# Kernel optimization log

Measured on AMD Instinct MI355X. Metric: run time of the kernel, lower is better.

The kernel has to match this reference:

```python
import jax, jax.numpy as jnp
import numpy as np

BATCH, SEQ, DMODEL, DHID = 4, 4096, 1024, 1024
R_MIN, R_MAX = 0.9, 0.99
MAX_PHASE = np.pi / 50  # module overrides ctor arg with pi/50
EPS = 1e-5


def setup_inputs() -> dict:
    key = jax.random.key(0)
    ks = jax.random.split(key, 8)
    # nu_init
    u1 = jax.random.uniform(ks[0], (DHID,)) * (1 - EPS) + EPS
    mag_sq = u1 * (R_MAX ** 2 - R_MIN ** 2) + R_MIN ** 2
    nu_log = jnp.log(-0.5 * jnp.log(mag_sq + EPS))
    # theta_init
    u2 = jax.random.uniform(ks[1], (DHID,)) * (1 - EPS) + EPS
    theta_log = jnp.log(MAX_PHASE * u2)
    B_re = jax.random.normal(ks[2], (DHID, DMODEL)) / np.sqrt(2 * DMODEL)
    B_im = jax.random.normal(ks[3], (DHID, DMODEL)) / np.sqrt(2 * DMODEL)
    C_re = jax.random.normal(ks[4], (DMODEL, DHID)) / np.sqrt(DHID)
    C_im = jax.random.normal(ks[5], (DMODEL, DHID)) / np.sqrt(DHID)
    D_skip = jax.random.normal(ks[6], (DMODEL,))
    inputs = jax.random.normal(ks[7], (BATCH, SEQ, DMODEL), dtype=jnp.float32)
    return {"inputs": inputs, "nu_log": nu_log, "theta_log": theta_log,
            "B_re": B_re, "B_im": B_im, "C_re": C_re, "C_im": C_im,
            "D_skip": D_skip}


def reference(inputs, nu_log, theta_log, B_re, B_im, C_re, C_im, D_skip):
    nu = jnp.exp(nu_log)
    theta = jnp.exp(theta_log)
    diag_lambda = jnp.exp(-nu + 1j * theta)            # [H] complex
    # forward recomputes gamma_log from nu_log (parameter gamma_log unused)
    gamma_log = 0.5 * jnp.log(1 - jnp.exp(-2 * jnp.exp(nu_log)) + EPS)
    B_norm = (B_re + 1j * B_im) * jnp.exp(gamma_log)[:, None]  # [H, D]
    inputs_c = inputs.astype(jnp.complex64)
    Bu = jnp.einsum('hd,btd->bth', B_norm, inputs_c)   # [B, T, H]

    def step(h, bu_t):
        h = diag_lambda * h + bu_t
        return h, h

    h0 = jnp.zeros((inputs.shape[0], diag_lambda.shape[0]), dtype=Bu.dtype)
    _, hs = jax.lax.scan(step, h0, jnp.swapaxes(Bu, 0, 1))  # [T, B, H]
    hs = jnp.swapaxes(hs, 0, 1)                              # [B, T, H]
    C_complex = C_re + 1j * C_im                              # [D, H]
    out = jnp.einsum('bth,dh->btd', hs, C_complex).real + inputs * D_skip
    return out.astype(jnp.float32)
```

## Files before the change

kernel.cpp:

```cpp
#include <hip/hip_runtime.h>


typedef __bf16 bf16x8 __attribute__((ext_vector_type(8)));
typedef float floatx4 __attribute__((ext_vector_type(4)));

__device__ __forceinline__ unsigned short f2bf(float f) {
  unsigned u = __float_as_uint(f);
  u += 0x7fffu + ((u >> 16) & 1u);
  return (unsigned short)(u >> 16);
}
__device__ __forceinline__ float bf2f(unsigned short s) {
  return __uint_as_float(((unsigned)s) << 16);
}


__global__ void prep_params(const float* __restrict__ nu_log,
                            const float* __restrict__ theta_log,
                            float* __restrict__ lam,
                            float* __restrict__ lamL,
                            float* __restrict__ gamma)
{
  int h = blockIdx.x * 256 + threadIdx.x;
  float nu = expf(nu_log[h]);
  float th = expf(theta_log[h]);
  float r = expf(-nu);
  lam[h]        = r * cosf(th);
  lam[1024 + h] = r * sinf(th);
  float rL = expf(-128.0f * nu);
  lamL[h]        = rL * cosf(128.0f * th);
  lamL[1024 + h] = rL * sinf(128.0f * th);
  gamma[h] = sqrtf(1.0f - expf(-2.0f * nu) + 1e-5f);
}

__global__ void prep_B(const float* __restrict__ B_re, const float* __restrict__ B_im,
                       const float* __restrict__ gamma, unsigned short* __restrict__ Bcat)
{
  int tid = blockIdx.x * 256 + threadIdx.x;
  int n = tid >> 10;
  int d = tid & 1023;
  int h = n & 1023;
  float v = (n < 1024 ? B_re[h * 1024 + d] : B_im[h * 1024 + d]) * gamma[h];
  Bcat[tid] = f2bf(v);
}

__global__ void prep_C(const float* __restrict__ C_re, const float* __restrict__ C_im,
                       unsigned short* __restrict__ Ccat)
{
  int tid = blockIdx.x * 256 + threadIdx.x;
  int d = tid >> 11;
  int k = tid & 2047;
  float v = (k < 1024) ? C_re[d * 1024 + k] : -C_im[d * 1024 + (k - 1024)];
  Ccat[tid] = f2bf(v);
}

__global__ void conv_inputs(const float* __restrict__ in, unsigned short* __restrict__ outb)
{
  int tid = blockIdx.x * 256 + threadIdx.x;
  float4 v = ((const float4*)in)[tid];
  unsigned lo = (unsigned)f2bf(v.x) | ((unsigned)f2bf(v.y) << 16);
  unsigned hi = (unsigned)f2bf(v.z) | ((unsigned)f2bf(v.w) << 16);
  ((uint2*)outb)[tid] = make_uint2(lo, hi);
}


template <int EPI>
__global__ __launch_bounds__(256) void gemm_bt_kernel(
    const unsigned short* __restrict__ A,
    const unsigned short* __restrict__ Bt,
    void* __restrict__ Cout,
    int M, int N, int K,
    const float* __restrict__ skip_in,
    const float* __restrict__ skip_w)
{
  __shared__ unsigned short As[2][128 * 32];
  __shared__ unsigned short Bs[2][128 * 32];

  const int tid  = threadIdx.x;
  const int lane = tid & 63;
  const int wave = tid >> 6;
  const int wm = wave >> 1;
  const int wn = wave & 1;

  const int flat    = blockIdx.x;
  const int xcd     = flat & 7;
  const int local   = flat >> 3;
  const int m_tile  = xcd * 16 + (local & 15);
  const int n_tile  = local >> 4;
  const int m0 = m_tile * 128;
  const int n0 = n_tile * 128;

  const int ldr = lane >> 2;
  const int pos = lane & 3;
  const int lm  = lane & 15;
  const int q   = lane >> 4;

  const int r0 = wave * 32 + ldr;
  const int ca0 = pos ^ ((r0 >> 1) & 3);
  const int r1 = r0 + 16;
  const int ca1 = pos ^ ((r1 >> 1) & 3);

  const unsigned short* gA0 = A  + (size_t)(m0 + r0) * K + ca0 * 8;
  const unsigned short* gA1 = A  + (size_t)(m0 + r1) * K + ca1 * 8;
  const unsigned short* gB0 = Bt + (size_t)(n0 + r0) * K + ca0 * 8;
  const unsigned short* gB1 = Bt + (size_t)(n0 + r1) * K + ca1 * 8;
  const int lofs0 = r0 * 32 + pos * 8;
  const int lofs1 = r1 * 32 + pos * 8;

  floatx4 acc[4][4];
#pragma unroll
  for (int i = 0; i < 4; ++i)
#pragma unroll
    for (int j = 0; j < 4; ++j)
      acc[i][j] = (floatx4){0.f, 0.f, 0.f, 0.f};

  {
    __builtin_amdgcn_global_load_lds(
        (const __attribute__((address_space(1))) void*)gA0,
        (__attribute__((address_space(3))) void*)&As[0][lofs0], 16, 0, 0);
    __builtin_amdgcn_global_load_lds(
        (const __attribute__((address_space(1))) void*)gA1,
        (__attribute__((address_space(3))) void*)&As[0][lofs1], 16, 0, 0);
    __builtin_amdgcn_global_load_lds(
        (const __attribute__((address_space(1))) void*)gB0,
        (__attribute__((address_space(3))) void*)&Bs[0][lofs0], 16, 0, 0);
    __builtin_amdgcn_global_load_lds(
        (const __attribute__((address_space(1))) void*)gB1,
        (__attribute__((address_space(3))) void*)&Bs[0][lofs1], 16, 0, 0);
  }

  int cur = 0;
  for (int kt = 0; kt < K; kt += 32) {
    __syncthreads();

    const int nxt = cur ^ 1;
    if (kt + 32 < K) {
      const int ko = kt + 32;
      __builtin_amdgcn_global_load_lds(
          (const __attribute__((address_space(1))) void*)(gA0 + ko),
          (__attribute__((address_space(3))) void*)&As[nxt][lofs0], 16, 0, 0);
      __builtin_amdgcn_global_load_lds(
          (const __attribute__((address_space(1))) void*)(gA1 + ko),
          (__attribute__((address_space(3))) void*)&As[nxt][lofs1], 16, 0, 0);
      __builtin_amdgcn_global_load_lds(
          (const __attribute__((address_space(1))) void*)(gB0 + ko),
          (__attribute__((address_space(3))) void*)&Bs[nxt][lofs0], 16, 0, 0);
      __builtin_amdgcn_global_load_lds(
          (const __attribute__((address_space(1))) void*)(gB1 + ko),
          (__attribute__((address_space(3))) void*)&Bs[nxt][lofs1], 16, 0, 0);
    }

    bf16x8 afrag[4], bfrag[4];
#pragma unroll
    for (int i = 0; i < 4; ++i) {
      const int r = wm * 64 + i * 16 + lm;
      afrag[i] = *reinterpret_cast<const bf16x8*>(&As[cur][r * 32 + (q ^ ((r >> 1) & 3)) * 8]);
    }
#pragma unroll
    for (int j = 0; j < 4; ++j) {
      const int r = wn * 64 + j * 16 + lm;
      bfrag[j] = *reinterpret_cast<const bf16x8*>(&Bs[cur][r * 32 + (q ^ ((r >> 1) & 3)) * 8]);
    }
#pragma unroll
    for (int i = 0; i < 4; ++i)
#pragma unroll
      for (int j = 0; j < 4; ++j)
        acc[i][j] = __builtin_amdgcn_mfma_f32_16x16x32_bf16(afrag[i], bfrag[j], acc[i][j], 0, 0, 0);

    cur = nxt;
  }

#pragma unroll
  for (int i = 0; i < 4; ++i) {
#pragma unroll
    for (int j = 0; j < 4; ++j) {
      const int row0 = m0 + wm * 64 + i * 16 + q * 4;
      const int col  = n0 + wn * 64 + j * 16 + lm;
#pragma unroll
      for (int r = 0; r < 4; ++r) {
        const size_t idx = (size_t)(row0 + r) * N + col;
        if (EPI == 0) {
          ((unsigned short*)Cout)[idx] = f2bf(acc[i][j][r]);
        } else {
          ((float*)Cout)[idx] = acc[i][j][r] + skip_in[idx] * skip_w[col];
        }
      }
    }
  }
}


__global__ void scan_finals(const unsigned short* __restrict__ Bu,
                            const float* __restrict__ lam,
                            float2* __restrict__ finals)
{
  int tid = blockIdx.x * 256 + threadIdx.x;
  int h = tid & 1023, c = (tid >> 10) & 31, b = tid >> 15;
  float lre = lam[h], lim = lam[1024 + h];
  const unsigned short* p = Bu + ((size_t)(b * 4096 + c * 128) * 2048) + h;
  float yre = 0.f, yim = 0.f;
#pragma unroll 4
  for (int t = 0; t < 128; ++t) {
    float ure = bf2f(p[0]);
    float uim = bf2f(p[1024]);
    float nre = fmaf(lre, yre, fmaf(-lim, yim, ure));
    float nim = fmaf(lre, yim, fmaf(lim, yre, uim));
    yre = nre; yim = nim;
    p += 2048;
  }
  finals[tid] = make_float2(yre, yim);
}

__global__ void scan_carries(const float2* __restrict__ finals,
                             const float* __restrict__ lamL,
                             float2* __restrict__ carry)
{
  int tid = blockIdx.x * 256 + threadIdx.x;
  int h = tid & 1023, b = tid >> 10;
  float Lre = lamL[h], Lim = lamL[1024 + h];
  float Hre = 0.f, Him = 0.f;
  for (int c = 0; c < 32; ++c) {
    size_t i = ((size_t)(b * 32 + c) << 10) + h;
    carry[i] = make_float2(Hre, Him);
    float2 f = finals[i];
    float nre = fmaf(Lre, Hre, fmaf(-Lim, Him, f.x));
    float nim = fmaf(Lre, Him, fmaf(Lim, Hre, f.y));
    Hre = nre; Him = nim;
  }
}

__global__ void scan_apply(const float* __restrict__ lam,
                           const float2* __restrict__ carry,
                           unsigned short* __restrict__ Bu)
{
  int tid = blockIdx.x * 256 + threadIdx.x;
  int h = tid & 1023, c = (tid >> 10) & 31, b = tid >> 15;
  float lre = lam[h], lim = lam[1024 + h];
  float2 cv = carry[tid];
  float yre = cv.x, yim = cv.y;
  unsigned short* p = Bu + ((size_t)(b * 4096 + c * 128) * 2048) + h;
#pragma unroll 4
  for (int t = 0; t < 128; ++t) {
    float ure = bf2f(p[0]);
    float uim = bf2f(p[1024]);
    float nre = fmaf(lre, yre, fmaf(-lim, yim, ure));
    float nim = fmaf(lre, yim, fmaf(lim, yre, uim));
    yre = nre; yim = nim;
    p[0]    = f2bf(yre);
    p[1024] = f2bf(yim);
    p += 2048;
  }
}


extern "C" void kernel_launch(void* const* d_in, const int* in_sizes, int n_in,
                              void* d_out, int out_size, void* d_ws, size_t ws_size,
                              hipStream_t stream)
{
  const float* inputs    = (const float*)d_in[0];
  const float* nu_log    = (const float*)d_in[1];
  const float* theta_log = (const float*)d_in[2];
  const float* B_re      = (const float*)d_in[3];
  const float* B_im      = (const float*)d_in[4];
  const float* C_re      = (const float*)d_in[5];
  const float* C_im      = (const float*)d_in[6];
  const float* D_skip    = (const float*)d_in[7];
  float* out = (float*)d_out;

  char* ws = (char*)d_ws;
  float* lam   = (float*)ws;
  float* lamL  = lam + 2048;
  float* gamma = lamL + 2048;
  unsigned short* inp_bf = (unsigned short*)(ws + (1 << 16));
  unsigned short* Bcat   = inp_bf + (size_t)16384 * 1024;
  unsigned short* Ccat   = Bcat   + (size_t)2048 * 1024;
  unsigned short* Bu     = Ccat   + (size_t)1024 * 2048;
  float2* finals = (float2*)(Bu + (size_t)16384 * 2048);
  float2* carry  = finals + 131072;

  prep_params<<<4,    256, 0, stream>>>(nu_log, theta_log, lam, lamL, gamma);
  prep_B     <<<8192, 256, 0, stream>>>(B_re, B_im, gamma, Bcat);
  prep_C     <<<8192, 256, 0, stream>>>(C_re, C_im, Ccat);
  conv_inputs<<<16384,256, 0, stream>>>(inputs, inp_bf);

  gemm_bt_kernel<0><<<2048, 256, 0, stream>>>(
      inp_bf, Bcat, Bu, 16384, 2048, 1024, nullptr, nullptr);

  scan_finals <<<512, 256, 0, stream>>>(Bu, lam, finals);
  scan_carries<<<16,  256, 0, stream>>>(finals, lamL, carry);
  scan_apply  <<<512, 256, 0, stream>>>(lam, carry, Bu);

  gemm_bt_kernel<1><<<1024, 256, 0, stream>>>(
      Bu, Ccat, out, 16384, 1024, 2048, inputs, D_skip);
}
```

Measured before the change: 364.2 us.

## Fuse prep kernels, load GEMM A fragments directly, vectorize scan kernels

Merges the four preprocessing kernels into one launch, with gamma computed inline per B element. The GEMM kernel now reads its A operand fragments straight from global memory into registers, skipping the LDS staging for A. The scan kernels handle four hidden channels per thread using 8-byte packed bf16 loads and stores, with a quarter of the blocks. This cuts launches, LDS traffic and per-element load count, but risks uncoalesced, unprefetched A reads in the GEMMs and lower occupancy in the scans (only 128 blocks).

Result: slower. 515.1 us (+41.4%).

```diff
diff --git a/kernel.cpp b/kernel.cpp
--- a/kernel.cpp
+++ b/kernel.cpp
@@ -14,52 +14,51 @@
 }
 
 
-__global__ void prep_params(const float* __restrict__ nu_log,
-                            const float* __restrict__ theta_log,
-                            float* __restrict__ lam,
-                            float* __restrict__ lamL,
-                            float* __restrict__ gamma)
-{
-  int h = blockIdx.x * 256 + threadIdx.x;
-  float nu = expf(nu_log[h]);
-  float th = expf(theta_log[h]);
-  float r = expf(-nu);
-  lam[h]        = r * cosf(th);
-  lam[1024 + h] = r * sinf(th);
-  float rL = expf(-128.0f * nu);
-  lamL[h]        = rL * cosf(128.0f * th);
-  lamL[1024 + h] = rL * sinf(128.0f * th);
-  gamma[h] = sqrtf(1.0f - expf(-2.0f * nu) + 1e-5f);
-}
-
-__global__ void prep_B(const float* __restrict__ B_re, const float* __restrict__ B_im,
-                       const float* __restrict__ gamma, unsigned short* __restrict__ Bcat)
-{
-  int tid = blockIdx.x * 256 + threadIdx.x;
-  int n = tid >> 10;
-  int d = tid & 1023;
-  int h = n & 1023;
-  float v = (n < 1024 ? B_re[h * 1024 + d] : B_im[h * 1024 + d]) * gamma[h];
-  Bcat[tid] = f2bf(v);
-}
-
-__global__ void prep_C(const float* __restrict__ C_re, const float* __restrict__ C_im,
-                       unsigned short* __restrict__ Ccat)
-{
-  int tid = blockIdx.x * 256 + threadIdx.x;
-  int d = tid >> 11;
-  int k = tid & 2047;
-  float v = (k < 1024) ? C_re[d * 1024 + k] : -C_im[d * 1024 + (k - 1024)];
-  Ccat[tid] = f2bf(v);
-}
-
-__global__ void conv_inputs(const float* __restrict__ in, unsigned short* __restrict__ outb)
-{
-  int tid = blockIdx.x * 256 + threadIdx.x;
-  float4 v = ((const float4*)in)[tid];
-  unsigned lo = (unsigned)f2bf(v.x) | ((unsigned)f2bf(v.y) << 16);
-  unsigned hi = (unsigned)f2bf(v.z) | ((unsigned)f2bf(v.w) << 16);
-  ((uint2*)outb)[tid] = make_uint2(lo, hi);
+__global__ void prep_fused(const float* __restrict__ nu_log,
+                           const float* __restrict__ theta_log,
+                           const float* __restrict__ B_re,
+                           const float* __restrict__ B_im,
+                           const float* __restrict__ C_re,
+                           const float* __restrict__ C_im,
+                           const float* __restrict__ inputs,
+                           float* __restrict__ lam,
+                           float* __restrict__ lamL,
+                           unsigned short* __restrict__ Bcat,
+                           unsigned short* __restrict__ Ccat,
+                           unsigned short* __restrict__ inp_bf)
+{
+  const int bx = blockIdx.x;
+  if (bx < 16384) {
+    int tid = bx * 256 + threadIdx.x;
+    float4 v = ((const float4*)inputs)[tid];
+    unsigned lo = (unsigned)f2bf(v.x) | ((unsigned)f2bf(v.y) << 16);
+    unsigned hi = (unsigned)f2bf(v.z) | ((unsigned)f2bf(v.w) << 16);
+    ((uint2*)inp_bf)[tid] = make_uint2(lo, hi);
+  } else if (bx < 24576) {
+    int tid = (bx - 16384) * 256 + threadIdx.x;
+    int n = tid >> 10;
+    int d = tid & 1023;
+    int h = n & 1023;
+    float gamma = sqrtf(1.0f - expf(-2.0f * expf(nu_log[h])) + 1e-5f);
+    float v = (n < 1024 ? B_re[h * 1024 + d] : B_im[h * 1024 + d]) * gamma;
+    Bcat[tid] = f2bf(v);
+  } else if (bx < 32768) {
+    int tid = (bx - 24576) * 256 + threadIdx.x;
+    int d = tid >> 11;
+    int k = tid & 2047;
+    float v = (k < 1024) ? C_re[d * 1024 + k] : -C_im[d * 1024 + (k - 1024)];
+    Ccat[tid] = f2bf(v);
+  } else {
+    int h = (bx - 32768) * 256 + threadIdx.x;
+    float nu = expf(nu_log[h]);
+    float th = expf(theta_log[h]);
+    float r = expf(-nu);
+    lam[h]        = r * cosf(th);
+    lam[1024 + h] = r * sinf(th);
+    float rL = expf(-128.0f * nu);
+    lamL[h]        = rL * cosf(128.0f * th);
+    lamL[1024 + h] = rL * sinf(128.0f * th);
+  }
 }
 
 
@@ -72,7 +71,6 @@
     const float* __restrict__ skip_in,
     const float* __restrict__ skip_w)
 {
-  __shared__ unsigned short As[2][128 * 32];
   __shared__ unsigned short Bs[2][128 * 32];
 
   const int tid  = threadIdx.x;
@@ -98,14 +96,13 @@
   const int ca0 = pos ^ ((r0 >> 1) & 3);
   const int r1 = r0 + 16;
   const int ca1 = pos ^ ((r1 >> 1) & 3);
-
-  const unsigned short* gA0 = A  + (size_t)(m0 + r0) * K + ca0 * 8;
-  const unsigned short* gA1 = A  + (size_t)(m0 + r1) * K + ca1 * 8;
   const unsigned short* gB0 = Bt + (size_t)(n0 + r0) * K + ca0 * 8;
   const unsigned short* gB1 = Bt + (size_t)(n0 + r1) * K + ca1 * 8;
   const int lofs0 = r0 * 32 + pos * 8;
   const int lofs1 = r1 * 32 + pos * 8;
 
+  const unsigned short* gAf = A + (size_t)(m0 + wm * 64 + lm) * K + q * 8;
+
   floatx4 acc[4][4];
 #pragma unroll
   for (int i = 0; i < 4; ++i)
@@ -113,20 +110,12 @@
     for (int j = 0; j < 4; ++j)
       acc[i][j] = (floatx4){0.f, 0.f, 0.f, 0.f};
 
-  {
-    __builtin_amdgcn_global_load_lds(
-        (const __attribute__((address_space(1))) void*)gA0,
-        (__attribute__((address_space(3))) void*)&As[0][lofs0], 16, 0, 0);
-    __builtin_amdgcn_global_load_lds(
-        (const __attribute__((address_space(1))) void*)gA1,
-        (__attribute__((address_space(3))) void*)&As[0][lofs1], 16, 0, 0);
-    __builtin_amdgcn_global_load_lds(
-        (const __attribute__((address_space(1))) void*)gB0,
-        (__attribute__((address_space(3))) void*)&Bs[0][lofs0], 16, 0, 0);
-    __builtin_amdgcn_global_load_lds(
-        (const __attribute__((address_space(1))) void*)gB1,
-        (__attribute__((address_space(3))) void*)&Bs[0][lofs1], 16, 0, 0);
-  }
+  __builtin_amdgcn_global_load_lds(
+      (const __attribute__((address_space(1))) void*)gB0,
+      (__attribute__((address_space(3))) void*)&Bs[0][lofs0], 16, 0, 0);
+  __builtin_amdgcn_global_load_lds(
+      (const __attribute__((address_space(1))) void*)gB1,
+      (__attribute__((address_space(3))) void*)&Bs[0][lofs1], 16, 0, 0);
 
   int cur = 0;
   for (int kt = 0; kt < K; kt += 32) {
@@ -135,12 +124,6 @@
     const int nxt = cur ^ 1;
     if (kt + 32 < K) {
       const int ko = kt + 32;
-      __builtin_amdgcn_global_load_lds(
-          (const __attribute__((address_space(1))) void*)(gA0 + ko),
-          (__attribute__((address_space(3))) void*)&As[nxt][lofs0], 16, 0, 0);
-      __builtin_amdgcn_global_load_lds(
-          (const __attribute__((address_space(1))) void*)(gA1 + ko),
-          (__attribute__((address_space(3))) void*)&As[nxt][lofs1], 16, 0, 0);
       __builtin_amdgcn_global_load_lds(
           (const __attribute__((address_space(1))) void*)(gB0 + ko),
           (__attribute__((address_space(3))) void*)&Bs[nxt][lofs0], 16, 0, 0);
@@ -149,17 +132,18 @@
           (__attribute__((address_space(3))) void*)&Bs[nxt][lofs1], 16, 0, 0);
     }
 
-    bf16x8 afrag[4], bfrag[4];
-#pragma unroll
-    for (int i = 0; i < 4; ++i) {
-      const int r = wm * 64 + i * 16 + lm;
-      afrag[i] = *reinterpret_cast<const bf16x8*>(&As[cur][r * 32 + (q ^ ((r >> 1) & 3)) * 8]);
-    }
+    bf16x8 afrag[4];
+#pragma unroll
+    for (int i = 0; i < 4; ++i)
+      afrag[i] = *reinterpret_cast<const bf16x8*>(gAf + (size_t)i * 16 * K + kt);
+
+    bf16x8 bfrag[4];
 #pragma unroll
     for (int j = 0; j < 4; ++j) {
       const int r = wn * 64 + j * 16 + lm;
       bfrag[j] = *reinterpret_cast<const bf16x8*>(&Bs[cur][r * 32 + (q ^ ((r >> 1) & 3)) * 8]);
     }
+
 #pragma unroll
     for (int i = 0; i < 4; ++i)
 #pragma unroll
@@ -194,20 +178,31 @@
                             float2* __restrict__ finals)
 {
   int tid = blockIdx.x * 256 + threadIdx.x;
-  int h = tid & 1023, c = (tid >> 10) & 31, b = tid >> 15;
-  float lre = lam[h], lim = lam[1024 + h];
-  const unsigned short* p = Bu + ((size_t)(b * 4096 + c * 128) * 2048) + h;
-  float yre = 0.f, yim = 0.f;
-#pragma unroll 4
+  int h4 = (tid & 255) * 4, c = (tid >> 8) & 31, b = tid >> 13;
+  float lre[4], lim[4], yre[4], yim[4];
+#pragma unroll
+  for (int j = 0; j < 4; ++j) {
+    lre[j] = lam[h4 + j]; lim[j] = lam[1024 + h4 + j];
+    yre[j] = 0.f; yim[j] = 0.f;
+  }
+  const unsigned short* p = Bu + ((size_t)(b * 4096 + c * 128) * 2048) + h4;
+#pragma unroll 2
   for (int t = 0; t < 128; ++t) {
-    float ure = bf2f(p[0]);
-    float uim = bf2f(p[1024]);
-    float nre = fmaf(lre, yre, fmaf(-lim, yim, ure));
-    float nim = fmaf(lre, yim, fmaf(lim, yre, uim));
-    yre = nre; yim = nim;
+    uint2 ur = *(const uint2*)(p);
+    uint2 ui = *(const uint2*)(p + 1024);
+    float re[4] = {bf2f(ur.x & 0xffff), bf2f(ur.x >> 16), bf2f(ur.y & 0xffff), bf2f(ur.y >> 16)};
+    float im[4] = {bf2f(ui.x & 0xffff), bf2f(ui.x >> 16), bf2f(ui.y & 0xffff), bf2f(ui.y >> 16)};
+#pragma unroll
+    for (int j = 0; j < 4; ++j) {
+      float nre = fmaf(lre[j], yre[j], fmaf(-lim[j], yim[j], re[j]));
+      float nim = fmaf(lre[j], yim[j], fmaf(lim[j], yre[j], im[j]));
+      yre[j] = nre; yim[j] = nim;
+    }
     p += 2048;
   }
-  finals[tid] = make_float2(yre, yim);
+  float2* f = finals + ((size_t)(b * 32 + c) << 10) + h4;
+#pragma unroll
+  for (int j = 0; j < 4; ++j) f[j] = make_float2(yre[j], yim[j]);
 }
 
 __global__ void scan_carries(const float2* __restrict__ finals,
@@ -233,20 +228,35 @@
                            unsigned short* __restrict__ Bu)
 {
   int tid = blockIdx.x * 256 + threadIdx.x;
-  int h = tid & 1023, c = (tid >> 10) & 31, b = tid >> 15;
-  float lre = lam[h], lim = lam[1024 + h];
-  float2 cv = carry[tid];
-  float yre = cv.x, yim = cv.y;
-  unsigned short* p = Bu + ((size_t)(b * 4096 + c * 128) * 2048) + h;
-#pragma unroll 4
+  int h4 = (tid & 255) * 4, c = (tid >> 8) & 31, b = tid >> 13;
+  float lre[4], lim[4], yre[4], yim[4];
+  const float2* cv = carry + ((size_t)(b * 32 + c) << 10) + h4;
+#pragma unroll
+  for (int j = 0; j < 4; ++j) {
+    lre[j] = lam[h4 + j]; lim[j] = lam[1024 + h4 + j];
+    float2 v = cv[j];
+    yre[j] = v.x; yim[j] = v.y;
+  }
+  unsigned short* p = Bu + ((size_t)(b * 4096 + c * 128) * 2048) + h4;
+#pragma unroll 2
   for (int t = 0; t < 128; ++t) {
-    float ure = bf2f(p[0]);
-    float uim = bf2f(p[1024]);
-    float nre = fmaf(lre, yre, fmaf(-lim, yim, ure));
-    float nim = fmaf(lre, yim, fmaf(lim, yre, uim));
-    yre = nre; yim = nim;
-    p[0]    = f2bf(yre);
-    p[1024] = f2bf(yim);
+    uint2 ur = *(const uint2*)(p);
+    uint2 ui = *(const uint2*)(p + 1024);
+    float re[4] = {bf2f(ur.x & 0xffff), bf2f(ur.x >> 16), bf2f(ur.y & 0xffff), bf2f(ur.y >> 16)};
+    float im[4] = {bf2f(ui.x & 0xffff), bf2f(ui.x >> 16), bf2f(ui.y & 0xffff), bf2f(ui.y >> 16)};
+#pragma unroll
+    for (int j = 0; j < 4; ++j) {
+      float nre = fmaf(lre[j], yre[j], fmaf(-lim[j], yim[j], re[j]));
+      float nim = fmaf(lre[j], yim[j], fmaf(lim[j], yre[j], im[j]));
+      yre[j] = nre; yim[j] = nim;
+    }
+    uint2 sr, si;
+    sr.x = (unsigned)f2bf(yre[0]) | ((unsigned)f2bf(yre[1]) << 16);
+    sr.y = (unsigned)f2bf(yre[2]) | ((unsigned)f2bf(yre[3]) << 16);
+    si.x = (unsigned)f2bf(yim[0]) | ((unsigned)f2bf(yim[1]) << 16);
+    si.y = (unsigned)f2bf(yim[2]) | ((unsigned)f2bf(yim[3]) << 16);
+    *(uint2*)(p) = sr;
+    *(uint2*)(p + 1024) = si;
     p += 2048;
   }
 }
@@ -269,7 +279,6 @@
   char* ws = (char*)d_ws;
   float* lam   = (float*)ws;
   float* lamL  = lam + 2048;
-  float* gamma = lamL + 2048;
   unsigned short* inp_bf = (unsigned short*)(ws + (1 << 16));
   unsigned short* Bcat   = inp_bf + (size_t)16384 * 1024;
   unsigned short* Ccat   = Bcat   + (size_t)2048 * 1024;
@@ -277,17 +286,15 @@
   float2* finals = (float2*)(Bu + (size_t)16384 * 2048);
   float2* carry  = finals + 131072;
 
-  prep_params<<<4,    256, 0, stream>>>(nu_log, theta_log, lam, lamL, gamma);
-  prep_B     <<<8192, 256, 0, stream>>>(B_re, B_im, gamma, Bcat);
-  prep_C     <<<8192, 256, 0, stream>>>(C_re, C_im, Ccat);
-  conv_inputs<<<16384,256, 0, stream>>>(inputs, inp_bf);
+  prep_fused<<<32772, 256, 0, stream>>>(nu_log, theta_log, B_re, B_im, C_re, C_im,
+                                        inputs, lam, lamL, Bcat, Ccat, inp_bf);
 
   gemm_bt_kernel<0><<<2048, 256, 0, stream>>>(
       inp_bf, Bcat, Bu, 16384, 2048, 1024, nullptr, nullptr);
 
-  scan_finals <<<512, 256, 0, stream>>>(Bu, lam, finals);
+  scan_finals <<<128, 256, 0, stream>>>(Bu, lam, finals);
   scan_carries<<<16,  256, 0, stream>>>(finals, lamL, carry);
-  scan_apply  <<<512, 256, 0, stream>>>(lam, carry, Bu);
+  scan_apply  <<<128, 256, 0, stream>>>(lam, carry, Bu);
 
   gemm_bt_kernel<1><<<1024, 256, 0, stream>>>(
       Bu, Ccat, out, 16384, 1024, 2048, inputs, D_skip);
```
